# Performance work log

Hardware: AMD Instinct MI355X
Metric: run time of the kernel (lower is better)

Reference implementation:

```python
import jax, jax.numpy as jnp
import numpy as np

COMMITMENT_COST = 0.25


def setup_inputs() -> dict:
    key = jax.random.key(0)
    k1, k2 = jax.random.split(key)
    inputs = jax.random.normal(k1, (64, 1024, 128), dtype=jnp.float32)
    # torch.rand init -> uniform [0, 1)
    codewords = jax.random.uniform(k2, (1024, 128), dtype=jnp.float32)
    return {"inputs": inputs, "codewords": codewords}


def reference(inputs, codewords):
    sg = jax.lax.stop_gradient
    D = codewords.shape[-1]
    flat = inputs.reshape(-1, D)  # (N, D)
    distances = (
        jnp.sum(flat * flat, axis=1, keepdims=True)
        - 2.0 * flat @ codewords.T
        + jnp.sum(codewords * codewords, axis=1)
    )  # (N, K)
    encoding_indices = jnp.argmin(distances, axis=1)  # (N,)
    quantized = codewords[encoding_indices].reshape(inputs.shape)

    quantizing_loss = jnp.mean((sg(quantized) - inputs) ** 2)
    commitment_loss = jnp.mean((quantized - sg(inputs)) ** 2)
    loss = quantizing_loss + COMMITMENT_COST * commitment_loss

    # straight-through estimator
    quantized = inputs + sg(quantized - inputs)
    return quantized, encoding_indices[:, None], loss
```

## Files before the change

### kernel.cpp

```cpp
#include <hip/hip_runtime.h>
#include <stdint.h>


typedef short     bf16x8 __attribute__((ext_vector_type(8)));
typedef float     f32x4  __attribute__((ext_vector_type(4)));
typedef unsigned short u16x8 __attribute__((ext_vector_type(8)));
typedef unsigned short u16x2 __attribute__((ext_vector_type(2)));

constexpr int N_ROWS = 65536;
constexpr int K_CODES = 1024;
constexpr int D = 128;
constexpr float MARGIN = 0.03f;

__device__ __forceinline__ unsigned short f32_to_bf16_rn(float f) {
    unsigned u = __float_as_uint(f);
    unsigned r = (u + 0x7FFFu + ((u >> 16) & 1u)) >> 16;
    return (unsigned short)r;
}
__device__ __forceinline__ float bf16_to_f32(unsigned short h) {
    return __uint_as_float(((unsigned)h) << 16);
}

__device__ __forceinline__ void gload_lds16(const void* g, void* l) {
    __builtin_amdgcn_global_load_lds(
        (const __attribute__((address_space(1))) unsigned int*)g,
        (__attribute__((address_space(3))) unsigned int*)l, 16, 0, 0);
}

__global__ __launch_bounds__(64) void vq_prep_cw(const float* __restrict__ cw,
                                                 unsigned short* __restrict__ Cp,
                                                 float* __restrict__ cnorm,
                                                 int* __restrict__ rcnt) {
    const int k = blockIdx.x;
    const int lane = threadIdx.x;
    float2 v = reinterpret_cast<const float2*>(cw + (size_t)k * D)[lane];
    float s = v.x * v.x + v.y * v.y;
#pragma unroll
    for (int off = 32; off; off >>= 1) s += __shfl_down(s, off, 64);
    if (lane == 0) cnorm[k] = s;
    if (lane == 0 && k == 0) *rcnt = 0;

    unsigned short hx = f32_to_bf16_rn(v.x), hy = f32_to_bf16_rn(v.y);
    unsigned short lx = f32_to_bf16_rn(v.x - bf16_to_f32(hx));
    unsigned short ly = f32_to_bf16_rn(v.y - bf16_to_f32(hy));
    size_t off0 = (size_t)k * D + lane * 2;
    u16x2 hv; hv[0] = hx; hv[1] = hy;
    u16x2 lv; lv[0] = lx; lv[1] = ly;
    *reinterpret_cast<u16x2*>(Cp + off0) = hv;
    *reinterpret_cast<u16x2*>(Cp + 131072 + off0) = lv;
}

__global__ __launch_bounds__(256, 2) void vq_argmin_mfma(
    const float* __restrict__ x,
    const unsigned short* __restrict__ Cp,
    const float* __restrict__ cnorm,
    float* __restrict__ out_idx_f,
    int* __restrict__ rcnt,
    int* __restrict__ repair_rows) {
    __shared__ unsigned char Bs[2][2][16384];

    const int tid = threadIdx.x;
    const int wave = tid >> 6;
    const int lane = tid & 63;
    const int l15 = lane & 15;
    const int lg = lane >> 4;
    const int wrow = blockIdx.x * 128 + wave * 32;

    const char* Cpb = reinterpret_cast<const char*>(Cp);
    auto stageB = [&](int c, int b) {
#pragma unroll
        for (int u = 0; u < 8; ++u) {
            int t = wave * 8 + u;
            int pl = t >> 4;
            int cwl = (t & 15) * 4 + lg;
            int q = l15 * 16;
            const char* src = Cpb + pl * 262144 + ((size_t)(c * 64 + cwl)) * 256
                              + (q ^ ((cwl & 7) << 4));
            void* dst = (void*)&Bs[b][pl][(t & 15) * 1024];
            gload_lds16(src, dst);
        }
    };
    stageB(0, 0);

    bf16x8 A[2][4][2];
#pragma unroll
    for (int r2 = 0; r2 < 2; ++r2) {
        const float* xr0 = x + (size_t)(wrow + r2 * 16 + l15) * D;
#pragma unroll
        for (int s = 0; s < 4; ++s) {
            const float4* xf = reinterpret_cast<const float4*>(xr0 + s * 32 + lg * 8);
            float4 f0 = xf[0];
            float4 f1 = xf[1];
            float in[8] = {f0.x, f0.y, f0.z, f0.w, f1.x, f1.y, f1.z, f1.w};
            u16x8 hv, lv;
#pragma unroll
            for (int e = 0; e < 8; ++e) {
                unsigned short h = f32_to_bf16_rn(in[e]);
                hv[e] = h;
                lv[e] = f32_to_bf16_rn(in[e] - bf16_to_f32(h));
            }
            A[r2][s][0] = *reinterpret_cast<bf16x8*>(&hv);
            A[r2][s][1] = *reinterpret_cast<bf16x8*>(&lv);
        }
    }

    float bv[2][4], bv2[2][4];
    int bi[2][4];
#pragma unroll
    for (int r2 = 0; r2 < 2; ++r2)
#pragma unroll
        for (int i = 0; i < 4; ++i) { bv[r2][i] = 3.4e38f; bv2[r2][i] = 3.4e38f; bi[r2][i] = 0; }

    const int cbase = l15 * 256;
    const int swz = (l15 & 7) << 4;
    int kb[4];
#pragma unroll
    for (int s = 0; s < 4; ++s) kb[s] = (s * 64 + lg * 16) ^ swz;

    asm volatile("s_waitcnt vmcnt(0)" ::: "memory");
    __syncthreads();

    for (int c = 0; c < 16; ++c) {
        const int buf = c & 1;
        if (c < 15) stageB(c + 1, buf ^ 1);

        f32x4 acc[2][4];
#pragma unroll
        for (int r2 = 0; r2 < 2; ++r2)
#pragma unroll
            for (int j = 0; j < 4; ++j) acc[r2][j] = (f32x4)(0.f);

#pragma unroll
        for (int s = 0; s < 4; ++s) {
            bf16x8 bh[4], bl[4];
#pragma unroll
            for (int j = 0; j < 4; ++j) {
                int ad = j * 4096 + cbase + kb[s];
                bh[j] = *reinterpret_cast<const bf16x8*>(&Bs[buf][0][ad]);
                bl[j] = *reinterpret_cast<const bf16x8*>(&Bs[buf][1][ad]);
            }
#pragma unroll
            for (int r2 = 0; r2 < 2; ++r2)
#pragma unroll
                for (int j = 0; j < 4; ++j) {
                    acc[r2][j] = __builtin_amdgcn_mfma_f32_16x16x32_bf16(
                        A[r2][s][0], bh[j], acc[r2][j], 0, 0, 0);
                    acc[r2][j] = __builtin_amdgcn_mfma_f32_16x16x32_bf16(
                        A[r2][s][0], bl[j], acc[r2][j], 0, 0, 0);
                    acc[r2][j] = __builtin_amdgcn_mfma_f32_16x16x32_bf16(
                        A[r2][s][1], bh[j], acc[r2][j], 0, 0, 0);
                }
        }

#pragma unroll
        for (int j = 0; j < 4; ++j) {
            int col = c * 64 + j * 16 + l15;
            float cn = cnorm[col];
#pragma unroll
            for (int r2 = 0; r2 < 2; ++r2)
#pragma unroll
                for (int i = 0; i < 4; ++i) {
                    float sc = cn - 2.f * acc[r2][j][i];
                    if (sc < bv[r2][i]) {
                        bv2[r2][i] = bv[r2][i];
                        bv[r2][i] = sc;
                        bi[r2][i] = col;
                    } else if (sc < bv2[r2][i]) {
                        bv2[r2][i] = sc;
                    }
                }
        }
        asm volatile("s_waitcnt vmcnt(0)" ::: "memory");
        __syncthreads();
    }

#pragma unroll
    for (int r2 = 0; r2 < 2; ++r2)
#pragma unroll
        for (int i = 0; i < 4; ++i) {
            float v = bv[r2][i], v2 = bv2[r2][i];
            int ix = bi[r2][i];
#pragma unroll
            for (int off = 1; off < 16; off <<= 1) {
                float ov = __shfl_xor(v, off, 64);
                float ov2 = __shfl_xor(v2, off, 64);
                int oi = __shfl_xor(ix, off, 64);
                float nv2 = fminf(fminf(v2, ov2), fmaxf(v, ov));
                if (ov < v || (ov == v && oi < ix)) { v = ov; ix = oi; }
                v2 = nv2;
            }
            if (l15 == 0) {
                int row = wrow + r2 * 16 + lg * 4 + i;
                out_idx_f[row] = (float)ix;
                if (v2 - v < MARGIN) {
                    int pos = atomicAdd(rcnt, 1);
                    repair_rows[pos] = row;
                }
            }
        }
}

__global__ __launch_bounds__(256) void vq_repair(const float* __restrict__ x,
                                                 const float* __restrict__ cw,
                                                 const float* __restrict__ cnorm,
                                                 const int* __restrict__ rcnt,
                                                 const int* __restrict__ repair_rows,
                                                 float* __restrict__ out_idx_f) {
    const int tid = threadIdx.x;
    const int count = *rcnt;
    __shared__ float xs[128];
    __shared__ float rv[4];
    __shared__ int ri[4];
    for (int w = blockIdx.x; w < count; w += 2048) {
        int row = repair_rows[w];
        if (w != (int)blockIdx.x) __syncthreads();
        if (tid < 32)
            reinterpret_cast<float4*>(xs)[tid] =
                reinterpret_cast<const float4*>(x + (size_t)row * D)[tid];
        __syncthreads();

        float bv = 3.4e38f;
        int bi = 0;
#pragma unroll
        for (int g = 0; g < 4; ++g) {
            int k = g * 256 + tid;
            const float4* cr = reinterpret_cast<const float4*>(cw + (size_t)k * D);
            float dot = 0.f;
#pragma unroll 8
            for (int d4 = 0; d4 < 32; ++d4) {
                float4 cv = cr[d4];
                float4 xv = reinterpret_cast<const float4*>(xs)[d4];
                dot += xv.x * cv.x;
                dot += xv.y * cv.y;
                dot += xv.z * cv.z;
                dot += xv.w * cv.w;
            }
            float sc = cnorm[k] - 2.f * dot;
            if (sc < bv) { bv = sc; bi = k; }
        }
#pragma unroll
        for (int off = 1; off < 64; off <<= 1) {
            float ov = __shfl_xor(bv, off, 64);
            int oi = __shfl_xor(bi, off, 64);
            if (ov < bv || (ov == bv && oi < bi)) { bv = ov; bi = oi; }
        }
        if ((tid & 63) == 0) { rv[tid >> 6] = bv; ri[tid >> 6] = bi; }
        __syncthreads();
        if (tid == 0) {
            float fv = rv[0];
            int fi = ri[0];
#pragma unroll
            for (int q = 1; q < 4; ++q)
                if (rv[q] < fv || (rv[q] == fv && ri[q] < fi)) { fv = rv[q]; fi = ri[q]; }
            out_idx_f[row] = (float)fi;
        }
    }
}

__global__ __launch_bounds__(256) void vq_gather_loss(const float* __restrict__ x,
                                                      const float* __restrict__ cw,
                                                      const float* __restrict__ idx_f,
                                                      float* __restrict__ qout,
                                                      double* __restrict__ partials) {
    const int total4 = N_ROWS * D / 4;
    double lsum = 0.0;
    for (int i = blockIdx.x * blockDim.x + threadIdx.x; i < total4;
         i += gridDim.x * blockDim.x) {
        int n = i >> 5;
        int d4 = i & 31;
        int k = (int)idx_f[n];
        float4 q = reinterpret_cast<const float4*>(cw + (size_t)k * D)[d4];
        float4 xv = reinterpret_cast<const float4*>(x)[i];
        float dxx = q.x - xv.x, dxy = q.y - xv.y, dxz = q.z - xv.z, dxw = q.w - xv.w;
        float4 o;
        o.x = xv.x + dxx; o.y = xv.y + dxy; o.z = xv.z + dxz; o.w = xv.w + dxw;
        reinterpret_cast<float4*>(qout)[i] = o;
        lsum += (double)(dxx * dxx + dxy * dxy + dxz * dxz + dxw * dxw);
    }
#pragma unroll
    for (int off = 32; off; off >>= 1) lsum += __shfl_down(lsum, off, 64);
    __shared__ double wsum[4];
    if ((threadIdx.x & 63) == 0) wsum[threadIdx.x >> 6] = lsum;
    __syncthreads();
    if (threadIdx.x == 0)
        partials[blockIdx.x] = wsum[0] + wsum[1] + wsum[2] + wsum[3];
}

__global__ __launch_bounds__(256) void vq_finalize(const double* __restrict__ partials,
                                                   float* __restrict__ out_loss) {
    double s = 0.0;
    for (int i = threadIdx.x; i < 2048; i += 256) s += partials[i];
#pragma unroll
    for (int off = 32; off; off >>= 1) s += __shfl_down(s, off, 64);
    __shared__ double wsum[4];
    if ((threadIdx.x & 63) == 0) wsum[threadIdx.x >> 6] = s;
    __syncthreads();
    if (threadIdx.x == 0)
        *out_loss = (float)((wsum[0] + wsum[1] + wsum[2] + wsum[3]) *
                            (1.25 / (double)((size_t)N_ROWS * D)));
}

extern "C" void kernel_launch(void* const* d_in, const int* in_sizes, int n_in,
                              void* d_out, int out_size, void* d_ws, size_t ws_size,
                              hipStream_t stream) {
    const float* x = (const float*)d_in[0];
    const float* cw = (const float*)d_in[1];

    float* qout = (float*)d_out;
    float* out_idx_f = qout + (size_t)N_ROWS * D;
    float* out_loss = out_idx_f + N_ROWS;

    char* rest;
    if (ws_size >= (2u << 20)) {
        rest = (char*)d_ws;
    } else {
        rest = (char*)qout;
    }
    unsigned short* Cp = (unsigned short*)rest;
    float* cnorm = (float*)(rest + 524288);
    int* rcnt = (int*)(rest + 524288 + 4096);
    int* rrows = (int*)(rest + 524288 + 4096 + 256);
    double* partials = (double*)(rest + 524288 + 4096 + 256 + 262144);

    vq_prep_cw<<<K_CODES, 64, 0, stream>>>(cw, Cp, cnorm, rcnt);
    vq_argmin_mfma<<<N_ROWS / 128, 256, 0, stream>>>(x, Cp, cnorm, out_idx_f, rcnt, rrows);
    vq_repair<<<2048, 256, 0, stream>>>(x, cw, cnorm, rcnt, rrows, out_idx_f);
    vq_gather_loss<<<2048, 256, 0, stream>>>(x, cw, out_idx_f, qout, partials);
    vq_finalize<<<1, 256, 0, stream>>>(partials, out_loss);
}
```

Measured before the change: 212.8 us.

## Split codebook across two blocks per tile and fuse gather with merge

The argmin kernel now launches two blocks per 128-row tile, each scanning half of the codebook with half the LDS footprint and higher occupancy. A new merge kernel combines the two partial best/second-best results, gathers the quantized rows, and computes the per-row loss analytically from ||x||^2 plus the best score. This avoids a separate full pass that re-read x for the loss. The repair kernel is batched to handle 16 rows per block and writes its corrections into the outputs, and the workspace now always lives in d_ws. The trade-offs are extra kernel launches, intermediate buffers, and a loss computed from the distance expansion rather than directly.

```diff
diff --git a/kernel.cpp b/kernel.cpp
--- a/kernel.cpp
+++ b/kernel.cpp
@@ -50,39 +50,43 @@
     *reinterpret_cast<u16x2*>(Cp + 131072 + off0) = lv;
 }
 
-__global__ __launch_bounds__(256, 2) void vq_argmin_mfma(
+__global__ __launch_bounds__(256, 3) void vq_argmin_mfma(
     const float* __restrict__ x,
     const unsigned short* __restrict__ Cp,
     const float* __restrict__ cnorm,
-    float* __restrict__ out_idx_f,
-    int* __restrict__ rcnt,
-    int* __restrict__ repair_rows) {
-    __shared__ unsigned char Bs[2][2][16384];
+    float* __restrict__ half_bv,
+    float* __restrict__ half_bv2,
+    int* __restrict__ half_bi,
+    float* __restrict__ xnorm) {
+    __shared__ unsigned char Bs[2][2][8192];
 
     const int tid = threadIdx.x;
     const int wave = tid >> 6;
     const int lane = tid & 63;
     const int l15 = lane & 15;
     const int lg = lane >> 4;
-    const int wrow = blockIdx.x * 128 + wave * 32;
+    const int tile = blockIdx.x >> 1;
+    const int khalf = blockIdx.x & 1;
+    const int wrow = tile * 128 + wave * 32;
 
     const char* Cpb = reinterpret_cast<const char*>(Cp);
     auto stageB = [&](int c, int b) {
 #pragma unroll
-        for (int u = 0; u < 8; ++u) {
-            int t = wave * 8 + u;
-            int pl = t >> 4;
-            int cwl = (t & 15) * 4 + lg;
+        for (int u = 0; u < 4; ++u) {
+            int t = wave * 4 + u;
+            int pl = t >> 3;
+            int cwl = (t & 7) * 4 + lg;
             int q = l15 * 16;
-            const char* src = Cpb + pl * 262144 + ((size_t)(c * 64 + cwl)) * 256
-                              + (q ^ ((cwl & 7) << 4));
-            void* dst = (void*)&Bs[b][pl][(t & 15) * 1024];
+            const char* src = Cpb + pl * 262144 + khalf * 131072
+                              + ((size_t)(c * 32 + cwl)) * 256 + (q ^ ((cwl & 7) << 4));
+            void* dst = (void*)&Bs[b][pl][(t & 7) * 1024];
             gload_lds16(src, dst);
         }
     };
     stageB(0, 0);
 
     bf16x8 A[2][4][2];
+    float xn[2] = {0.f, 0.f};
 #pragma unroll
     for (int r2 = 0; r2 < 2; ++r2) {
         const float* xr0 = x + (size_t)(wrow + r2 * 16 + l15) * D;
@@ -95,6 +99,7 @@
             u16x8 hv, lv;
 #pragma unroll
             for (int e = 0; e < 8; ++e) {
+                xn[r2] += in[e] * in[e];
                 unsigned short h = f32_to_bf16_rn(in[e]);
                 hv[e] = h;
                 lv[e] = f32_to_bf16_rn(in[e] - bf16_to_f32(h));
@@ -103,15 +108,21 @@
             A[r2][s][1] = *reinterpret_cast<bf16x8*>(&lv);
         }
     }
+#pragma unroll
+    for (int r2 = 0; r2 < 2; ++r2) {
+        xn[r2] += __shfl_xor(xn[r2], 16, 64);
+        xn[r2] += __shfl_xor(xn[r2], 32, 64);
+        if (khalf == 0 && lg == 0) xnorm[wrow + r2 * 16 + l15] = xn[r2];
+    }
 
     float bv[2][4], bv2[2][4];
-    int bi[2][4];
+    int bi_[2][4];
 #pragma unroll
     for (int r2 = 0; r2 < 2; ++r2)
 #pragma unroll
-        for (int i = 0; i < 4; ++i) { bv[r2][i] = 3.4e38f; bv2[r2][i] = 3.4e38f; bi[r2][i] = 0; }
-
-    const int cbase = l15 * 256;
+        for (int i = 0; i < 4; ++i) { bv[r2][i] = 3.4e38f; bv2[r2][i] = 3.4e38f; bi_[r2][i] = 0; }
+
+    const int cb = l15 * 256;
     const int swz = (l15 & 7) << 4;
     int kb[4];
 #pragma unroll
@@ -124,25 +135,25 @@
         const int buf = c & 1;
         if (c < 15) stageB(c + 1, buf ^ 1);
 
-        f32x4 acc[2][4];
+        f32x4 acc[2][2];
 #pragma unroll
         for (int r2 = 0; r2 < 2; ++r2)
 #pragma unroll
-            for (int j = 0; j < 4; ++j) acc[r2][j] = (f32x4)(0.f);
+            for (int j = 0; j < 2; ++j) acc[r2][j] = (f32x4)(0.f);
 
 #pragma unroll
         for (int s = 0; s < 4; ++s) {
-            bf16x8 bh[4], bl[4];
-#pragma unroll
-            for (int j = 0; j < 4; ++j) {
-                int ad = j * 4096 + cbase + kb[s];
+            bf16x8 bh[2], bl[2];
+#pragma unroll
+            for (int j = 0; j < 2; ++j) {
+                int ad = j * 4096 + cb + kb[s];
                 bh[j] = *reinterpret_cast<const bf16x8*>(&Bs[buf][0][ad]);
                 bl[j] = *reinterpret_cast<const bf16x8*>(&Bs[buf][1][ad]);
             }
 #pragma unroll
             for (int r2 = 0; r2 < 2; ++r2)
 #pragma unroll
-                for (int j = 0; j < 4; ++j) {
+                for (int j = 0; j < 2; ++j) {
                     acc[r2][j] = __builtin_amdgcn_mfma_f32_16x16x32_bf16(
                         A[r2][s][0], bh[j], acc[r2][j], 0, 0, 0);
                     acc[r2][j] = __builtin_amdgcn_mfma_f32_16x16x32_bf16(
@@ -153,8 +164,8 @@
         }
 
 #pragma unroll
-        for (int j = 0; j < 4; ++j) {
-            int col = c * 64 + j * 16 + l15;
+        for (int j = 0; j < 2; ++j) {
+            int col = khalf * 512 + c * 32 + j * 16 + l15;
             float cn = cnorm[col];
 #pragma unroll
             for (int r2 = 0; r2 < 2; ++r2)
@@ -164,7 +175,7 @@
                     if (sc < bv[r2][i]) {
                         bv2[r2][i] = bv[r2][i];
                         bv[r2][i] = sc;
-                        bi[r2][i] = col;
+                        bi_[r2][i] = col;
                     } else if (sc < bv2[r2][i]) {
                         bv2[r2][i] = sc;
                     }
@@ -179,7 +190,7 @@
 #pragma unroll
         for (int i = 0; i < 4; ++i) {
             float v = bv[r2][i], v2 = bv2[r2][i];
-            int ix = bi[r2][i];
+            int ix = bi_[r2][i];
 #pragma unroll
             for (int off = 1; off < 16; off <<= 1) {
                 float ov = __shfl_xor(v, off, 64);
@@ -191,113 +202,148 @@
             }
             if (l15 == 0) {
                 int row = wrow + r2 * 16 + lg * 4 + i;
-                out_idx_f[row] = (float)ix;
-                if (v2 - v < MARGIN) {
-                    int pos = atomicAdd(rcnt, 1);
-                    repair_rows[pos] = row;
-                }
-            }
-        }
+                int o = khalf * N_ROWS + row;
+                half_bv[o] = v;
+                half_bv2[o] = v2;
+                half_bi[o] = ix;
+            }
+        }
+}
+
+__global__ __launch_bounds__(256) void vq_merge(const float* __restrict__ cw,
+                                                const float* __restrict__ half_bv,
+                                                const float* __restrict__ half_bv2,
+                                                const int* __restrict__ half_bi,
+                                                const float* __restrict__ xnorm,
+                                                float* __restrict__ out_idx_f,
+                                                float* __restrict__ qout,
+                                                float* __restrict__ rowloss,
+                                                int* __restrict__ rcnt,
+                                                int* __restrict__ rrows) {
+    const int t = threadIdx.x;
+    const int row = blockIdx.x * 8 + (t >> 5);
+    const int d4 = t & 31;
+
+    float v0 = half_bv[row], v0b = half_bv2[row];
+    int i0 = half_bi[row];
+    float v1 = half_bv[N_ROWS + row], v1b = half_bv2[N_ROWS + row];
+    int i1 = half_bi[N_ROWS + row];
+
+    bool take0 = (v0 < v1) || (v0 == v1 && i0 <= i1);
+    float best = take0 ? v0 : v1;
+    int bidx = take0 ? i0 : i1;
+    float second = take0 ? fminf(v1, v0b) : fminf(v0, v1b);
+
+    float4 q4 = reinterpret_cast<const float4*>(cw)[(size_t)bidx * 32 + d4];
+    reinterpret_cast<float4*>(qout)[(size_t)row * 32 + d4] = q4;
+
+    if (d4 == 0) {
+        out_idx_f[row] = (float)bidx;
+        rowloss[row] = xnorm[row] + best;
+        if (second - best < MARGIN) {
+            int p = atomicAdd(rcnt, 1);
+            rrows[p] = row;
+        }
+    }
 }
 
 __global__ __launch_bounds__(256) void vq_repair(const float* __restrict__ x,
                                                  const float* __restrict__ cw,
                                                  const float* __restrict__ cnorm,
+                                                 const float* __restrict__ xnorm,
                                                  const int* __restrict__ rcnt,
-                                                 const int* __restrict__ repair_rows,
-                                                 float* __restrict__ out_idx_f) {
-    const int tid = threadIdx.x;
+                                                 const int* __restrict__ rrows,
+                                                 float* __restrict__ out_idx_f,
+                                                 float* __restrict__ qout,
+                                                 float* __restrict__ rowloss) {
+    __shared__ float xs[16][132];
+    __shared__ int rowids[16];
+    __shared__ float sval[16][16];
+    __shared__ int sidx[16][16];
+    __shared__ int fidx[16];
+
+    const int t = threadIdx.x;
     const int count = *rcnt;
-    __shared__ float xs[128];
-    __shared__ float rv[4];
-    __shared__ int ri[4];
-    for (int w = blockIdx.x; w < count; w += 2048) {
-        int row = repair_rows[w];
-        if (w != (int)blockIdx.x) __syncthreads();
-        if (tid < 32)
-            reinterpret_cast<float4*>(xs)[tid] =
-                reinterpret_cast<const float4*>(x + (size_t)row * D)[tid];
-        __syncthreads();
-
+    const float4* cw4 = reinterpret_cast<const float4*>(cw);
+
+    for (int g = blockIdx.x; g * 16 < count; g += 256) {
+        int nrows = min(16, count - g * 16);
+        __syncthreads();
+        if (t < 16) rowids[t] = rrows[g * 16 + (t < nrows ? t : 0)];
+        __syncthreads();
+        for (int i = t; i < 512; i += 256) {
+            int r = i >> 5, d4 = i & 31;
+            *reinterpret_cast<float4*>(&xs[r][d4 * 4]) =
+                reinterpret_cast<const float4*>(x)[(size_t)rowids[r] * 32 + d4];
+        }
+        __syncthreads();
+
+        const int r = t & 15;
+        const int qq = t >> 4;
         float bv = 3.4e38f;
         int bi = 0;
-#pragma unroll
-        for (int g = 0; g < 4; ++g) {
-            int k = g * 256 + tid;
-            const float4* cr = reinterpret_cast<const float4*>(cw + (size_t)k * D);
-            float dot = 0.f;
-#pragma unroll 8
+#pragma unroll 2
+        for (int kt = 0; kt < 8; ++kt) {
+            float a[8] = {0.f, 0.f, 0.f, 0.f, 0.f, 0.f, 0.f, 0.f};
+            int k0 = qq * 64 + kt * 8;
             for (int d4 = 0; d4 < 32; ++d4) {
-                float4 cv = cr[d4];
-                float4 xv = reinterpret_cast<const float4*>(xs)[d4];
-                dot += xv.x * cv.x;
-                dot += xv.y * cv.y;
-                dot += xv.z * cv.z;
-                dot += xv.w * cv.w;
-            }
-            float sc = cnorm[k] - 2.f * dot;
-            if (sc < bv) { bv = sc; bi = k; }
-        }
-#pragma unroll
-        for (int off = 1; off < 64; off <<= 1) {
-            float ov = __shfl_xor(bv, off, 64);
-            int oi = __shfl_xor(bi, off, 64);
-            if (ov < bv || (ov == bv && oi < bi)) { bv = ov; bi = oi; }
-        }
-        if ((tid & 63) == 0) { rv[tid >> 6] = bv; ri[tid >> 6] = bi; }
-        __syncthreads();
-        if (tid == 0) {
-            float fv = rv[0];
-            int fi = ri[0];
-#pragma unroll
-            for (int q = 1; q < 4; ++q)
-                if (rv[q] < fv || (rv[q] == fv && ri[q] < fi)) { fv = rv[q]; fi = ri[q]; }
-            out_idx_f[row] = (float)fi;
-        }
-    }
-}
-
-__global__ __launch_bounds__(256) void vq_gather_loss(const float* __restrict__ x,
-                                                      const float* __restrict__ cw,
-                                                      const float* __restrict__ idx_f,
-                                                      float* __restrict__ qout,
-                                                      double* __restrict__ partials) {
-    const int total4 = N_ROWS * D / 4;
-    double lsum = 0.0;
-    for (int i = blockIdx.x * blockDim.x + threadIdx.x; i < total4;
-         i += gridDim.x * blockDim.x) {
-        int n = i >> 5;
-        int d4 = i & 31;
-        int k = (int)idx_f[n];
-        float4 q = reinterpret_cast<const float4*>(cw + (size_t)k * D)[d4];
-        float4 xv = reinterpret_cast<const float4*>(x)[i];
-        float dxx = q.x - xv.x, dxy = q.y - xv.y, dxz = q.z - xv.z, dxw = q.w - xv.w;
-        float4 o;
-        o.x = xv.x + dxx; o.y = xv.y + dxy; o.z = xv.z + dxz; o.w = xv.w + dxw;
-        reinterpret_cast<float4*>(qout)[i] = o;
-        lsum += (double)(dxx * dxx + dxy * dxy + dxz * dxz + dxw * dxw);
-    }
-#pragma unroll
-    for (int off = 32; off; off >>= 1) lsum += __shfl_down(lsum, off, 64);
-    __shared__ double wsum[4];
-    if ((threadIdx.x & 63) == 0) wsum[threadIdx.x >> 6] = lsum;
-    __syncthreads();
-    if (threadIdx.x == 0)
-        partials[blockIdx.x] = wsum[0] + wsum[1] + wsum[2] + wsum[3];
-}
-
-__global__ __launch_bounds__(256) void vq_finalize(const double* __restrict__ partials,
-                                                   float* __restrict__ out_loss) {
+                float4 xv = *reinterpret_cast<const float4*>(&xs[r][d4 * 4]);
+#pragma unroll
+                for (int kk = 0; kk < 8; ++kk) {
+                    float4 cv = cw4[(size_t)(k0 + kk) * 32 + d4];
+                    a[kk] += xv.x * cv.x + xv.y * cv.y + xv.z * cv.z + xv.w * cv.w;
+                }
+            }
+#pragma unroll
+            for (int kk = 0; kk < 8; ++kk) {
+                int k = k0 + kk;
+                float sc = cnorm[k] - 2.f * a[kk];
+                if (sc < bv) { bv = sc; bi = k; }
+            }
+        }
+        sval[r][qq] = bv;
+        sidx[r][qq] = bi;
+        __syncthreads();
+        if (t < 16) {
+            float fv = sval[t][0];
+            int fi = sidx[t][0];
+#pragma unroll
+            for (int q2 = 1; q2 < 16; ++q2) {
+                float v = sval[t][q2];
+                int ii = sidx[t][q2];
+                if (v < fv || (v == fv && ii < fi)) { fv = v; fi = ii; }
+            }
+            fidx[t] = fi;
+            if (t < nrows) {
+                int row = rowids[t];
+                out_idx_f[row] = (float)fi;
+                rowloss[row] = xnorm[row] + fv;
+            }
+        }
+        __syncthreads();
+        for (int i = t; i < 512; i += 256) {
+            int rr = i >> 5, d4 = i & 31;
+            float4 q4 = cw4[(size_t)fidx[rr] * 32 + d4];
+            reinterpret_cast<float4*>(qout)[(size_t)rowids[rr] * 32 + d4] = q4;
+        }
+    }
+}
+
+__global__ __launch_bounds__(1024) void vq_loss_final(const float* __restrict__ rowloss,
+                                                      float* __restrict__ out_loss) {
     double s = 0.0;
-    for (int i = threadIdx.x; i < 2048; i += 256) s += partials[i];
+    for (int i = threadIdx.x; i < N_ROWS; i += 1024) s += (double)rowloss[i];
 #pragma unroll
     for (int off = 32; off; off >>= 1) s += __shfl_down(s, off, 64);
-    __shared__ double wsum[4];
+    __shared__ double wsum[16];
     if ((threadIdx.x & 63) == 0) wsum[threadIdx.x >> 6] = s;
     __syncthreads();
-    if (threadIdx.x == 0)
-        *out_loss = (float)((wsum[0] + wsum[1] + wsum[2] + wsum[3]) *
-                            (1.25 / (double)((size_t)N_ROWS * D)));
+    if (threadIdx.x == 0) {
+        double tot = 0.0;
+#pragma unroll
+        for (int i = 0; i < 16; ++i) tot += wsum[i];
+        *out_loss = (float)(tot * (1.25 / (double)((size_t)N_ROWS * D)));
+    }
 }
 
 extern "C" void kernel_launch(void* const* d_in, const int* in_sizes, int n_in,
@@ -310,21 +356,23 @@
     float* out_idx_f = qout + (size_t)N_ROWS * D;
     float* out_loss = out_idx_f + N_ROWS;
 
-    char* rest;
-    if (ws_size >= (2u << 20)) {
-        rest = (char*)d_ws;
-    } else {
-        rest = (char*)qout;
-    }
-    unsigned short* Cp = (unsigned short*)rest;
-    float* cnorm = (float*)(rest + 524288);
-    int* rcnt = (int*)(rest + 524288 + 4096);
-    int* rrows = (int*)(rest + 524288 + 4096 + 256);
-    double* partials = (double*)(rest + 524288 + 4096 + 256 + 262144);
+    char* w = (char*)d_ws;
+    unsigned short* Cp = (unsigned short*)w;          w += 524288;
+    float* cnorm = (float*)w;                         w += 4096;
+    int* rcnt = (int*)w;                              w += 256;
+    int* rrows = (int*)w;                             w += 262144;
+    float* half_bv = (float*)w;                       w += 524288;
+    float* half_bv2 = (float*)w;                      w += 524288;
+    int* half_bi = (int*)w;                           w += 524288;
+    float* xnorm = (float*)w;                         w += 262144;
+    float* rowloss = (float*)w;                       w += 262144;
 
     vq_prep_cw<<<K_CODES, 64, 0, stream>>>(cw, Cp, cnorm, rcnt);
-    vq_argmin_mfma<<<N_ROWS / 128, 256, 0, stream>>>(x, Cp, cnorm, out_idx_f, rcnt, rrows);
-    vq_repair<<<2048, 256, 0, stream>>>(x, cw, cnorm, rcnt, rrows, out_idx_f);
-    vq_gather_loss<<<2048, 256, 0, stream>>>(x, cw, out_idx_f, qout, partials);
-    vq_finalize<<<1, 256, 0, stream>>>(partials, out_loss);
-}
+    vq_argmin_mfma<<<(N_ROWS / 128) * 2, 256, 0, stream>>>(
+        x, Cp, cnorm, half_bv, half_bv2, half_bi, xnorm);
+    vq_merge<<<N_ROWS / 8, 256, 0, stream>>>(
+        cw, half_bv, half_bv2, half_bi, xnorm, out_idx_f, qout, rowloss, rcnt, rrows);
+    vq_repair<<<256, 256, 0, stream>>>(
+        x, cw, cnorm, xnorm, rcnt, rrows, out_idx_f, qout, rowloss);
+    vq_loss_final<<<1, 1024, 0, stream>>>(rowloss, out_loss);
+}
```

New measurement: 256.5 us. 1.21x slower.
